# Performance work log

Measured on AMD Instinct MI355X. Metric: run time of the kernel, lower is better.

Reference implementation:

```python
import jax, jax.numpy as jnp
import numpy as np

B = 1048576
H = 16  # LSTM hidden size

def setup_inputs() -> dict:
    key = jax.random.key(0)
    ks = jax.random.split(key, 16)
    s = 1.0 / np.sqrt(H)
    return {
        "mobility": jax.random.normal(ks[0], (B, 7, 1), dtype=jnp.float32),
        "controls": jax.random.normal(ks[1], (B, 5), dtype=jnp.float32),
        "last": jax.random.normal(ks[2], (B, 1), dtype=jnp.float32),
        # cc: Linear(5 -> 3)
        "W_cc": jax.random.uniform(ks[3], (3, 5), jnp.float32, -s, s),
        "b_cc": jax.random.uniform(ks[4], (3,), jnp.float32, -s, s),
        # LSTM(input=1, hidden=16), gate order i,f,g,o
        "W_ih": jax.random.uniform(ks[5], (4 * H, 1), jnp.float32, -s, s),
        "W_hh": jax.random.uniform(ks[6], (4 * H, H), jnp.float32, -s, s),
        "b_ih": jax.random.uniform(ks[7], (4 * H,), jnp.float32, -s, s),
        "b_hh": jax.random.uniform(ks[8], (4 * H,), jnp.float32, -s, s),
        # fc: Linear(19->16), Tanh, Dropout(eval=identity), Linear(16->16), Tanh, Linear(16->1), ReLU
        "W1": jax.random.uniform(ks[9], (16, 19), jnp.float32, -s, s),
        "b1": jax.random.uniform(ks[10], (16,), jnp.float32, -s, s),
        "W2": jax.random.uniform(ks[11], (16, 16), jnp.float32, -s, s),
        "b2": jax.random.uniform(ks[12], (16,), jnp.float32, -s, s),
        "W3": jax.random.uniform(ks[13], (1, 16), jnp.float32, -s, s),
        "b3": jax.random.uniform(ks[14], (1,), jnp.float32, -s, s),
    }

def _lstm(x, W_ih, W_hh, b_ih, b_hh):
    # x: [B, T, 1] -> final hidden state [B, H]
    b = x.shape[0]
    h0 = jnp.zeros((b, H), x.dtype)
    c0 = jnp.zeros((b, H), x.dtype)
    bias = b_ih + b_hh

    def step(carry, x_t):
        h, c = carry
        gates = x_t @ W_ih.T + h @ W_hh.T + bias  # [B, 4H]
        i, f, g, o = jnp.split(gates, 4, axis=-1)
        i = jax.nn.sigmoid(i)
        f = jax.nn.sigmoid(f)
        g = jnp.tanh(g)
        o = jax.nn.sigmoid(o)
        c = f * c + i * g
        h = o * jnp.tanh(c)
        return (h, c), None

    (h, c), _ = jax.lax.scan(step, (h0, c0), jnp.swapaxes(x, 0, 1))
    return h

def reference(mobility, controls, last, W_cc, b_cc, W_ih, W_hh, b_ih, b_hh, W1, b1, W2, b2, W3, b3):
    control = controls @ W_cc.T + b_cc                 # [B, 3]
    m = _lstm(mobility, W_ih, W_hh, b_ih, b_hh)        # [B, 16] final hidden
    x = jnp.concatenate([m, control], axis=1)          # [B, 19]
    x = jnp.tanh(x @ W1.T + b1)                        # dropout is identity (eval)
    x = jnp.tanh(x @ W2.T + b2)
    out = jax.nn.relu(x @ W3.T + b3)                   # [B, 1]
    return out
```

## Files before the change

kernel.cpp:

```cpp
#include <hip/hip_runtime.h>
#include <hip/hip_bf16.h>

typedef _Float16 f16x8  __attribute__((ext_vector_type(8)));
typedef _Float16 f16x16 __attribute__((ext_vector_type(16)));
typedef float    f32x16 __attribute__((ext_vector_type(16)));
typedef float    v2f    __attribute__((ext_vector_type(2)));
typedef unsigned u32x4  __attribute__((ext_vector_type(4)));

#define LOG2E 1.442695040888963f

__device__ __forceinline__ unsigned pk16(float a, float b) {
    return __builtin_bit_cast(unsigned, __builtin_amdgcn_cvt_pkrtz(a, b));
}

__global__ __launch_bounds__(256, 3) void lstm_mfma_kernel(
    const float* __restrict__ mobility,
    const float* __restrict__ controls,
    const float* __restrict__ W_cc, const float* __restrict__ b_cc,
    const float* __restrict__ W_ih, const float* __restrict__ W_hh,
    const float* __restrict__ b_ih, const float* __restrict__ b_hh,
    const float* __restrict__ W1,  const float* __restrict__ b1,
    const float* __restrict__ W2,  const float* __restrict__ b2,
    const float* __restrict__ W3,  const float* __restrict__ b3,
    float* __restrict__ out, int Btot)
{
    __shared__ float hbuf[256][17];
    __shared__ float mobs[256][7];

    const int tid  = threadIdx.x;
    const int lane = tid & 63;
    const int wib  = tid >> 6;
    const int col  = lane & 31;
    const int hi   = lane >> 5;

    const int blockRow0 = blockIdx.x * 256;

    {
        float* dst = &mobs[wib * 64][0];
        const float* src = mobility + (size_t)(blockRow0 + wib * 64) * 7;
        #pragma unroll
        for (int j = 0; j < 7; ++j) dst[lane + j * 64] = src[lane + j * 64];
    }

    f16x8 afrag[2];
    #pragma unroll
    for (int gb = 0; gb < 2; ++gb) {
        const float s = (gb == 0) ? -LOG2E : ((col < 16) ? 2.0f * LOG2E : -LOG2E);
        const float* wr = W_hh + (gb * 32 + col) * 16 + hi * 8;
        u32x4 aw = { pk16(s * wr[0], s * wr[1]), pk16(s * wr[2], s * wr[3]),
                     pk16(s * wr[4], s * wr[5]), pk16(s * wr[6], s * wr[7]) };
        afrag[gb] = __builtin_bit_cast(f16x8, aw);
    }

    f16x16 bias_h[2], wih_h[2];
    #pragma unroll
    for (int gb = 0; gb < 2; ++gb)
        #pragma unroll
        for (int q = 0; q < 4; ++q) {
            const int gu = gb * 32 + 8 * q + 4 * hi;
            const float s = (gu < 32) ? -LOG2E : ((gu < 48) ? 2.0f * LOG2E : -LOG2E);
            #pragma unroll
            for (int e = 0; e < 4; ++e) {
                bias_h[gb][4 * q + e] = (_Float16)(s * (b_ih[gu + e] + b_hh[gu + e]));
                wih_h [gb][4 * q + e] = (_Float16)(s * W_ih[gu + e]);
            }
        }

    float c[2][8];
    #pragma unroll
    for (int rb = 0; rb < 2; ++rb)
        #pragma unroll
        for (int u = 0; u < 8; ++u) c[rb][u] = 0.0f;

    u32x4 bz = { 0u, 0u, 0u, 0u };
    f16x8 bfrag[2];
    bfrag[0] = __builtin_bit_cast(f16x8, bz);
    bfrag[1] = __builtin_bit_cast(f16x8, bz);

    #pragma unroll 1
    for (int t = 0; t < 7; ++t) {
        #pragma unroll
        for (int rb = 0; rb < 2; ++rb) {
            const float xt = mobs[wib * 64 + col + rb * 32][t];

            f32x16 cin0, cin1;
            #pragma unroll
            for (int r = 0; r < 16; ++r)
                cin0[r] = fmaf(xt, (float)wih_h[0][r], (float)bias_h[0][r]);
            f32x16 a0 = __builtin_amdgcn_mfma_f32_32x32x16_f16(afrag[0], bfrag[rb], cin0, 0, 0, 0);
            #pragma unroll
            for (int r = 0; r < 16; ++r)
                cin1[r] = fmaf(xt, (float)wih_h[1][r], (float)bias_h[1][r]);
            f32x16 a1 = __builtin_amdgcn_mfma_f32_32x32x16_f16(afrag[1], bfrag[rb], cin1, 0, 0, 0);

            float h[8];
            #pragma unroll
            for (int u = 0; u < 8; u += 2) {
                const float ea0 = __builtin_amdgcn_exp2f(a0[u]);
                const float ef0 = __builtin_amdgcn_exp2f(a0[u + 8]);
                const float eb0 = __builtin_amdgcn_exp2f(a1[u]);
                const float eo0 = __builtin_amdgcn_exp2f(a1[u + 8]);
                const float ea1 = __builtin_amdgcn_exp2f(a0[u + 1]);
                const float ef1 = __builtin_amdgcn_exp2f(a0[u + 9]);
                const float eb1 = __builtin_amdgcn_exp2f(a1[u + 1]);
                const float eo1 = __builtin_amdgcn_exp2f(a1[u + 9]);

                const float pf0 = 1.0f + ef0, pa0 = 1.0f + ea0;
                const float pf1 = 1.0f + ef1, pa1 = 1.0f + ea1;
                const float den0 = fmaf(pa0, eb0, pa0);
                const float den1 = fmaf(pa1, eb1, pa1);
                const float D0 = den0 * pf0, D1 = den1 * pf1;
                const float num0 = fmaf(eb0, 2.0f * LOG2E, -2.0f * LOG2E);
                const float num1 = fmaf(eb1, 2.0f * LOG2E, -2.0f * LOG2E);
                const float cn0 = fmaf(c[rb][u],     den0, num0 * pf0);
                const float cn1 = fmaf(c[rb][u + 1], den1, num1 * pf1);
                const float rC = __builtin_amdgcn_rcpf(D0 * D1);
                const float cs0 = (cn0 * D1) * rC;
                const float cs1 = (cn1 * D0) * rC;
                c[rb][u]     = cs0;
                c[rb][u + 1] = cs1;
                const float ec0 = __builtin_amdgcn_exp2f(cs0);
                const float ec1 = __builtin_amdgcn_exp2f(cs1);
                const float ph0 = 1.0f + eo0, ph1 = 1.0f + eo1;
                const float dh0 = fmaf(ph0, ec0, ph0);
                const float dh1 = fmaf(ph1, ec1, ph1);
                const float rP = __builtin_amdgcn_rcpf(dh0 * dh1);
                h[u]     = ((ec0 - 1.0f) * dh1) * rP;
                h[u + 1] = ((ec1 - 1.0f) * dh0) * rP;
            }
            unsigned q0 = pk16(h[0], h[1]);
            unsigned q1 = pk16(h[2], h[3]);
            unsigned q2 = pk16(h[4], h[5]);
            unsigned q3 = pk16(h[6], h[7]);
            auto s02 = __builtin_amdgcn_permlane32_swap(q0, q2, false, false);
            auto s13 = __builtin_amdgcn_permlane32_swap(q1, q3, false, false);
            u32x4 bw = { s02[0], s13[0], s02[1], s13[1] };
            bfrag[rb] = __builtin_bit_cast(f16x8, bw);

            __builtin_amdgcn_sched_barrier(0);
        }
    }

    #pragma unroll
    for (int rb = 0; rb < 2; ++rb) {
        const int rr = wib * 64 + col + rb * 32;
        #pragma unroll
        for (int e = 0; e < 8; ++e)
            hbuf[rr][hi * 8 + e] = (float)bfrag[rb][e];
    }
    __syncthreads();

    const int grow = blockRow0 + tid;

    float x19[19];
    #pragma unroll
    for (int k = 0; k < 16; ++k) x19[k] = hbuf[tid][k];

    float ctl[5];
    #pragma unroll
    for (int k = 0; k < 5; ++k) ctl[k] = controls[grow * 5 + k];
    #pragma unroll
    for (int j = 0; j < 3; ++j) {
        float a = b_cc[j];
        #pragma unroll
        for (int k = 0; k < 5; ++k) a = fmaf(ctl[k], W_cc[j * 5 + k], a);
        x19[16 + j] = a;
    }

    float d1[16];
    #pragma unroll
    for (int j = 0; j < 16; ++j) {
        float a = b1[j];
        #pragma unroll
        for (int k = 0; k < 19; ++k) a = fmaf(x19[k], W1[j * 19 + k], a);
        d1[j] = __builtin_amdgcn_exp2f((2.0f * LOG2E) * a) + 1.0f;
    }
    v2f t12[8];
    #pragma unroll
    for (int j = 0; j < 16; j += 2) {
        const float rP = __builtin_amdgcn_rcpf(d1[j] * d1[j + 1]);
        t12[j >> 1][0] = fmaf(-2.0f * d1[j + 1], rP, 1.0f);
        t12[j >> 1][1] = fmaf(-2.0f * d1[j],     rP, 1.0f);
    }

    float d2[16];
    #pragma unroll
    for (int j = 0; j < 16; ++j) {
        const v2f* w2row = (const v2f*)(W2 + j * 16);
        v2f a = t12[0] * w2row[0];
        #pragma unroll
        for (int p = 1; p < 8; ++p) a = __builtin_elementwise_fma(t12[p], w2row[p], a);
        d2[j] = __builtin_amdgcn_exp2f((2.0f * LOG2E) * (a.x + a.y + b2[j])) + 1.0f;
    }
    v2f t22[8];
    #pragma unroll
    for (int j = 0; j < 16; j += 2) {
        const float rP = __builtin_amdgcn_rcpf(d2[j] * d2[j + 1]);
        t22[j >> 1][0] = fmaf(-2.0f * d2[j + 1], rP, 1.0f);
        t22[j >> 1][1] = fmaf(-2.0f * d2[j],     rP, 1.0f);
    }

    const v2f* w3p = (const v2f*)W3;
    v2f a3 = t22[0] * w3p[0];
    #pragma unroll
    for (int p = 1; p < 8; ++p) a3 = __builtin_elementwise_fma(t22[p], w3p[p], a3);
    const float r = a3.x + a3.y + b3[0];
    if (grow < Btot) out[grow] = fmaxf(r, 0.0f);
}

extern "C" void kernel_launch(void* const* d_in, const int* in_sizes, int n_in,
                              void* d_out, int out_size, void* d_ws, size_t ws_size,
                              hipStream_t stream) {
    const float* mobility = (const float*)d_in[0];
    const float* controls = (const float*)d_in[1];
    const float* W_cc = (const float*)d_in[3];
    const float* b_cc = (const float*)d_in[4];
    const float* W_ih = (const float*)d_in[5];
    const float* W_hh = (const float*)d_in[6];
    const float* b_ih = (const float*)d_in[7];
    const float* b_hh = (const float*)d_in[8];
    const float* W1   = (const float*)d_in[9];
    const float* b1   = (const float*)d_in[10];
    const float* W2   = (const float*)d_in[11];
    const float* b2   = (const float*)d_in[12];
    const float* W3   = (const float*)d_in[13];
    const float* b3   = (const float*)d_in[14];
    float* out = (float*)d_out;

    const int Btot = in_sizes[0] / 7;
    const int grid = (Btot + 255) / 256;

    lstm_mfma_kernel<<<grid, 256, 0, stream>>>(
        mobility, controls, W_cc, b_cc, W_ih, W_hh, b_ih, b_hh,
        W1, b1, W2, b2, W3, b3, out, Btot);
}
```

Before: 117.8 us.

## Halve rows per block to one 32-row MFMA tile per wave, raise occupancy

Each wave now handles a single 32-row tile through the LSTM recurrence instead of two interleaved tiles. Blocks cover 128 rows, the grid doubles, and launch bounds target 4 blocks per CU. This cuts register pressure and raises occupancy. In exchange it gives up the within-wave ILP from the two independent recurrence chains, and half the threads sit idle in the MLP epilogue.

```diff
diff --git a/kernel.cpp b/kernel.cpp
--- a/kernel.cpp
+++ b/kernel.cpp
@@ -13,7 +13,7 @@
     return __builtin_bit_cast(unsigned, __builtin_amdgcn_cvt_pkrtz(a, b));
 }
 
-__global__ __launch_bounds__(256, 3) void lstm_mfma_kernel(
+__global__ __launch_bounds__(256, 4) void lstm_mfma_kernel(
     const float* __restrict__ mobility,
     const float* __restrict__ controls,
     const float* __restrict__ W_cc, const float* __restrict__ b_cc,
@@ -24,8 +24,8 @@
     const float* __restrict__ W3,  const float* __restrict__ b3,
     float* __restrict__ out, int Btot)
 {
-    __shared__ float hbuf[256][17];
-    __shared__ float mobs[256][7];
+    __shared__ float hbuf[128][17];
+    __shared__ float mobs[128][7];
 
     const int tid  = threadIdx.x;
     const int lane = tid & 63;
@@ -33,13 +33,16 @@
     const int col  = lane & 31;
     const int hi   = lane >> 5;
 
-    const int blockRow0 = blockIdx.x * 256;
+    const int blockRow0 = blockIdx.x * 128;
 
     {
-        float* dst = &mobs[wib * 64][0];
-        const float* src = mobility + (size_t)(blockRow0 + wib * 64) * 7;
-        #pragma unroll
-        for (int j = 0; j < 7; ++j) dst[lane + j * 64] = src[lane + j * 64];
+        float* dst = &mobs[wib * 32][0];
+        const float* src = mobility + (size_t)(blockRow0 + wib * 32) * 7;
+        #pragma unroll
+        for (int j = 0; j < 4; ++j) {
+            const int i = lane + j * 64;
+            if (i < 224) dst[i] = src[i];
+        }
     }
 
     f16x8 afrag[2];
@@ -66,146 +69,138 @@
             }
         }
 
-    float c[2][8];
+    float c[8];
     #pragma unroll
-    for (int rb = 0; rb < 2; ++rb)
-        #pragma unroll
-        for (int u = 0; u < 8; ++u) c[rb][u] = 0.0f;
+    for (int u = 0; u < 8; ++u) c[u] = 0.0f;
 
     u32x4 bz = { 0u, 0u, 0u, 0u };
-    f16x8 bfrag[2];
-    bfrag[0] = __builtin_bit_cast(f16x8, bz);
-    bfrag[1] = __builtin_bit_cast(f16x8, bz);
+    f16x8 bfrag = __builtin_bit_cast(f16x8, bz);
 
     #pragma unroll 1
     for (int t = 0; t < 7; ++t) {
-        #pragma unroll
-        for (int rb = 0; rb < 2; ++rb) {
-            const float xt = mobs[wib * 64 + col + rb * 32][t];
-
-            f32x16 cin0, cin1;
-            #pragma unroll
-            for (int r = 0; r < 16; ++r)
-                cin0[r] = fmaf(xt, (float)wih_h[0][r], (float)bias_h[0][r]);
-            f32x16 a0 = __builtin_amdgcn_mfma_f32_32x32x16_f16(afrag[0], bfrag[rb], cin0, 0, 0, 0);
-            #pragma unroll
-            for (int r = 0; r < 16; ++r)
-                cin1[r] = fmaf(xt, (float)wih_h[1][r], (float)bias_h[1][r]);
-            f32x16 a1 = __builtin_amdgcn_mfma_f32_32x32x16_f16(afrag[1], bfrag[rb], cin1, 0, 0, 0);
-
-            float h[8];
-            #pragma unroll
-            for (int u = 0; u < 8; u += 2) {
-                const float ea0 = __builtin_amdgcn_exp2f(a0[u]);
-                const float ef0 = __builtin_amdgcn_exp2f(a0[u + 8]);
-                const float eb0 = __builtin_amdgcn_exp2f(a1[u]);
-                const float eo0 = __builtin_amdgcn_exp2f(a1[u + 8]);
-                const float ea1 = __builtin_amdgcn_exp2f(a0[u + 1]);
-                const float ef1 = __builtin_amdgcn_exp2f(a0[u + 9]);
-                const float eb1 = __builtin_amdgcn_exp2f(a1[u + 1]);
-                const float eo1 = __builtin_amdgcn_exp2f(a1[u + 9]);
-
-                const float pf0 = 1.0f + ef0, pa0 = 1.0f + ea0;
-                const float pf1 = 1.0f + ef1, pa1 = 1.0f + ea1;
-                const float den0 = fmaf(pa0, eb0, pa0);
-                const float den1 = fmaf(pa1, eb1, pa1);
-                const float D0 = den0 * pf0, D1 = den1 * pf1;
-                const float num0 = fmaf(eb0, 2.0f * LOG2E, -2.0f * LOG2E);
-                const float num1 = fmaf(eb1, 2.0f * LOG2E, -2.0f * LOG2E);
-                const float cn0 = fmaf(c[rb][u],     den0, num0 * pf0);
-                const float cn1 = fmaf(c[rb][u + 1], den1, num1 * pf1);
-                const float rC = __builtin_amdgcn_rcpf(D0 * D1);
-                const float cs0 = (cn0 * D1) * rC;
-                const float cs1 = (cn1 * D0) * rC;
-                c[rb][u]     = cs0;
-                c[rb][u + 1] = cs1;
-                const float ec0 = __builtin_amdgcn_exp2f(cs0);
-                const float ec1 = __builtin_amdgcn_exp2f(cs1);
-                const float ph0 = 1.0f + eo0, ph1 = 1.0f + eo1;
-                const float dh0 = fmaf(ph0, ec0, ph0);
-                const float dh1 = fmaf(ph1, ec1, ph1);
-                const float rP = __builtin_amdgcn_rcpf(dh0 * dh1);
-                h[u]     = ((ec0 - 1.0f) * dh1) * rP;
-                h[u + 1] = ((ec1 - 1.0f) * dh0) * rP;
-            }
-            unsigned q0 = pk16(h[0], h[1]);
-            unsigned q1 = pk16(h[2], h[3]);
-            unsigned q2 = pk16(h[4], h[5]);
-            unsigned q3 = pk16(h[6], h[7]);
-            auto s02 = __builtin_amdgcn_permlane32_swap(q0, q2, false, false);
-            auto s13 = __builtin_amdgcn_permlane32_swap(q1, q3, false, false);
-            u32x4 bw = { s02[0], s13[0], s02[1], s13[1] };
-            bfrag[rb] = __builtin_bit_cast(f16x8, bw);
-
-            __builtin_amdgcn_sched_barrier(0);
-        }
-    }
-
-    #pragma unroll
-    for (int rb = 0; rb < 2; ++rb) {
-        const int rr = wib * 64 + col + rb * 32;
+        const float xt = mobs[wib * 32 + col][t];
+
+        f32x16 cin0, cin1;
+        #pragma unroll
+        for (int r = 0; r < 16; ++r)
+            cin0[r] = fmaf(xt, (float)wih_h[0][r], (float)bias_h[0][r]);
+        f32x16 a0 = __builtin_amdgcn_mfma_f32_32x32x16_f16(afrag[0], bfrag, cin0, 0, 0, 0);
+        #pragma unroll
+        for (int r = 0; r < 16; ++r)
+            cin1[r] = fmaf(xt, (float)wih_h[1][r], (float)bias_h[1][r]);
+        f32x16 a1 = __builtin_amdgcn_mfma_f32_32x32x16_f16(afrag[1], bfrag, cin1, 0, 0, 0);
+
+        float h[8];
+        #pragma unroll
+        for (int u = 0; u < 8; u += 2) {
+            const float ea0 = __builtin_amdgcn_exp2f(a0[u]);
+            const float ef0 = __builtin_amdgcn_exp2f(a0[u + 8]);
+            const float eb0 = __builtin_amdgcn_exp2f(a1[u]);
+            const float eo0 = __builtin_amdgcn_exp2f(a1[u + 8]);
+            const float ea1 = __builtin_amdgcn_exp2f(a0[u + 1]);
+            const float ef1 = __builtin_amdgcn_exp2f(a0[u + 9]);
+            const float eb1 = __builtin_amdgcn_exp2f(a1[u + 1]);
+            const float eo1 = __builtin_amdgcn_exp2f(a1[u + 9]);
+
+            const float pf0 = 1.0f + ef0, pa0 = 1.0f + ea0;
+            const float pf1 = 1.0f + ef1, pa1 = 1.0f + ea1;
+            const float den0 = fmaf(pa0, eb0, pa0);
+            const float den1 = fmaf(pa1, eb1, pa1);
+            const float D0 = den0 * pf0, D1 = den1 * pf1;
+            const float num0 = fmaf(eb0, 2.0f * LOG2E, -2.0f * LOG2E);
+            const float num1 = fmaf(eb1, 2.0f * LOG2E, -2.0f * LOG2E);
+            const float cn0 = fmaf(c[u],     den0, num0 * pf0);
+            const float cn1 = fmaf(c[u + 1], den1, num1 * pf1);
+            const float rC = __builtin_amdgcn_rcpf(D0 * D1);
+            const float cs0 = (cn0 * D1) * rC;
+            const float cs1 = (cn1 * D0) * rC;
+            c[u]     = cs0;
+            c[u + 1] = cs1;
+            const float ec0 = __builtin_amdgcn_exp2f(cs0);
+            const float ec1 = __builtin_amdgcn_exp2f(cs1);
+            const float ph0 = 1.0f + eo0, ph1 = 1.0f + eo1;
+            const float dh0 = fmaf(ph0, ec0, ph0);
+            const float dh1 = fmaf(ph1, ec1, ph1);
+            const float rP = __builtin_amdgcn_rcpf(dh0 * dh1);
+            h[u]     = ((ec0 - 1.0f) * dh1) * rP;
+            h[u + 1] = ((ec1 - 1.0f) * dh0) * rP;
+        }
+        unsigned q0 = pk16(h[0], h[1]);
+        unsigned q1 = pk16(h[2], h[3]);
+        unsigned q2 = pk16(h[4], h[5]);
+        unsigned q3 = pk16(h[6], h[7]);
+        auto s02 = __builtin_amdgcn_permlane32_swap(q0, q2, false, false);
+        auto s13 = __builtin_amdgcn_permlane32_swap(q1, q3, false, false);
+        u32x4 bw = { s02[0], s13[0], s02[1], s13[1] };
+        bfrag = __builtin_bit_cast(f16x8, bw);
+    }
+
+    {
+        const int rr = wib * 32 + col;
         #pragma unroll
         for (int e = 0; e < 8; ++e)
-            hbuf[rr][hi * 8 + e] = (float)bfrag[rb][e];
+            hbuf[rr][hi * 8 + e] = (float)bfrag[e];
     }
     __syncthreads();
 
-    const int grow = blockRow0 + tid;
-
-    float x19[19];
-    #pragma unroll
-    for (int k = 0; k < 16; ++k) x19[k] = hbuf[tid][k];
-
-    float ctl[5];
-    #pragma unroll
-    for (int k = 0; k < 5; ++k) ctl[k] = controls[grow * 5 + k];
-    #pragma unroll
-    for (int j = 0; j < 3; ++j) {
-        float a = b_cc[j];
-        #pragma unroll
-        for (int k = 0; k < 5; ++k) a = fmaf(ctl[k], W_cc[j * 5 + k], a);
-        x19[16 + j] = a;
-    }
-
-    float d1[16];
-    #pragma unroll
-    for (int j = 0; j < 16; ++j) {
-        float a = b1[j];
-        #pragma unroll
-        for (int k = 0; k < 19; ++k) a = fmaf(x19[k], W1[j * 19 + k], a);
-        d1[j] = __builtin_amdgcn_exp2f((2.0f * LOG2E) * a) + 1.0f;
-    }
-    v2f t12[8];
-    #pragma unroll
-    for (int j = 0; j < 16; j += 2) {
-        const float rP = __builtin_amdgcn_rcpf(d1[j] * d1[j + 1]);
-        t12[j >> 1][0] = fmaf(-2.0f * d1[j + 1], rP, 1.0f);
-        t12[j >> 1][1] = fmaf(-2.0f * d1[j],     rP, 1.0f);
-    }
-
-    float d2[16];
-    #pragma unroll
-    for (int j = 0; j < 16; ++j) {
-        const v2f* w2row = (const v2f*)(W2 + j * 16);
-        v2f a = t12[0] * w2row[0];
-        #pragma unroll
-        for (int p = 1; p < 8; ++p) a = __builtin_elementwise_fma(t12[p], w2row[p], a);
-        d2[j] = __builtin_amdgcn_exp2f((2.0f * LOG2E) * (a.x + a.y + b2[j])) + 1.0f;
-    }
-    v2f t22[8];
-    #pragma unroll
-    for (int j = 0; j < 16; j += 2) {
-        const float rP = __builtin_amdgcn_rcpf(d2[j] * d2[j + 1]);
-        t22[j >> 1][0] = fmaf(-2.0f * d2[j + 1], rP, 1.0f);
-        t22[j >> 1][1] = fmaf(-2.0f * d2[j],     rP, 1.0f);
-    }
-
-    const v2f* w3p = (const v2f*)W3;
-    v2f a3 = t22[0] * w3p[0];
-    #pragma unroll
-    for (int p = 1; p < 8; ++p) a3 = __builtin_elementwise_fma(t22[p], w3p[p], a3);
-    const float r = a3.x + a3.y + b3[0];
-    if (grow < Btot) out[grow] = fmaxf(r, 0.0f);
+    if (tid < 128) {
+        const int grow = blockRow0 + tid;
+
+        float x19[19];
+        #pragma unroll
+        for (int k = 0; k < 16; ++k) x19[k] = hbuf[tid][k];
+
+        float ctl[5];
+        #pragma unroll
+        for (int k = 0; k < 5; ++k) ctl[k] = controls[grow * 5 + k];
+        #pragma unroll
+        for (int j = 0; j < 3; ++j) {
+            float a = b_cc[j];
+            #pragma unroll
+            for (int k = 0; k < 5; ++k) a = fmaf(ctl[k], W_cc[j * 5 + k], a);
+            x19[16 + j] = a;
+        }
+
+        float d1[16];
+        #pragma unroll
+        for (int j = 0; j < 16; ++j) {
+            float a = b1[j];
+            #pragma unroll
+            for (int k = 0; k < 19; ++k) a = fmaf(x19[k], W1[j * 19 + k], a);
+            d1[j] = __builtin_amdgcn_exp2f((2.0f * LOG2E) * a) + 1.0f;
+        }
+        v2f t12[8];
+        #pragma unroll
+        for (int j = 0; j < 16; j += 2) {
+            const float rP = __builtin_amdgcn_rcpf(d1[j] * d1[j + 1]);
+            t12[j >> 1][0] = fmaf(-2.0f * d1[j + 1], rP, 1.0f);
+            t12[j >> 1][1] = fmaf(-2.0f * d1[j],     rP, 1.0f);
+        }
+
+        float d2[16];
+        #pragma unroll
+        for (int j = 0; j < 16; ++j) {
+            const v2f* w2row = (const v2f*)(W2 + j * 16);
+            v2f a = t12[0] * w2row[0];
+            #pragma unroll
+            for (int p = 1; p < 8; ++p) a = __builtin_elementwise_fma(t12[p], w2row[p], a);
+            d2[j] = __builtin_amdgcn_exp2f((2.0f * LOG2E) * (a.x + a.y + b2[j])) + 1.0f;
+        }
+        v2f t22[8];
+        #pragma unroll
+        for (int j = 0; j < 16; j += 2) {
+            const float rP = __builtin_amdgcn_rcpf(d2[j] * d2[j + 1]);
+            t22[j >> 1][0] = fmaf(-2.0f * d2[j + 1], rP, 1.0f);
+            t22[j >> 1][1] = fmaf(-2.0f * d2[j],     rP, 1.0f);
+        }
+
+        const v2f* w3p = (const v2f*)W3;
+        v2f a3 = t22[0] * w3p[0];
+        #pragma unroll
+        for (int p = 1; p < 8; ++p) a3 = __builtin_elementwise_fma(t22[p], w3p[p], a3);
+        const float r = a3.x + a3.y + b3[0];
+        if (grow < Btot) out[grow] = fmaxf(r, 0.0f);
+    }
 }
 
 extern "C" void kernel_launch(void* const* d_in, const int* in_sizes, int n_in,
@@ -228,7 +223,7 @@
     float* out = (float*)d_out;
 
     const int Btot = in_sizes[0] / 7;
-    const int grid = (Btot + 255) / 256;
+    const int grid = (Btot + 127) / 128;
 
     lstm_mfma_kernel<<<grid, 256, 0, stream>>>(
         mobility, controls, W_cc, b_cc, W_ih, W_hh, b_ih, b_hh,
```

Result: slower. 123.8 us (+5.1%).
